# Kernel optimization log

Hardware: AMD Instinct MI355X
Metric: run time of the kernel (lower is better)

The kernel has to match this reference:

```python
import jax, jax.numpy as jnp
import numpy as np

B, C, L, H = 4, 512, 2048, 8
D = C // H  # head_dim


def setup_inputs() -> dict:
    key = jax.random.key(0)
    ks = jax.random.split(key, 9)
    s = 1.0 / np.sqrt(C)  # keep logits well-scaled like torch Linear init
    return {
        "x": jax.random.normal(ks[0], (B, C, L), dtype=jnp.float32),
        "Wq": jax.random.normal(ks[1], (C, C), dtype=jnp.float32) * s,
        "bq": jnp.zeros((C,), dtype=jnp.float32),
        "Wk": jax.random.normal(ks[2], (C, C), dtype=jnp.float32) * s,
        "bk": jnp.zeros((C,), dtype=jnp.float32),
        "Wv": jax.random.normal(ks[3], (C, C), dtype=jnp.float32) * s,
        "bv": jnp.zeros((C,), dtype=jnp.float32),
        "Wo": jax.random.normal(ks[4], (C, C), dtype=jnp.float32) * s,
        "bo": jnp.zeros((C,), dtype=jnp.float32),
    }


def reference(x, Wq, bq, Wk, bk, Wv, bv, Wo, bo):
    # x: (B, C, L) -> (B, L, C)
    xp = jnp.transpose(x, (0, 2, 1))
    scale = D ** (-0.5)

    def heads(w, b):
        y = xp @ w.T + b                      # (B, L, C)  torch Linear: x W^T + b
        return y.reshape(B, L, H, D).transpose(0, 2, 1, 3)  # (B, H, L, D)

    q = heads(Wq, bq)
    k = heads(Wk, bk)
    v = heads(Wv, bv)

    attn = jnp.einsum('bhqd,bhkd->bhqk', q, k) * scale  # (B, H, L, L)
    attn = jax.nn.softmax(attn, axis=-1)
    out = jnp.einsum('bhqk,bhkd->bhqd', attn, v)        # (B, H, L, D)
    out = out.transpose(0, 2, 1, 3).reshape(B, L, C)    # (B, L, C)
    out = out @ Wo.T + bo
    return x + jnp.transpose(out, (0, 2, 1))            # residual in (B, C, L)
```

## Files before the change

kernel.cpp:

```cpp
#include <hip/hip_runtime.h>
#include <math.h>

#define B_ 4
#define C_ 512
#define L_ 2048
#define H_ 8
#define D_ 64
#define QSCALE 0.18033688011112042f
#define DEFER_THR 12.0f

typedef __bf16 bf16x8 __attribute__((ext_vector_type(8)));
typedef float f32x4 __attribute__((ext_vector_type(4)));

__device__ __forceinline__ unsigned short f2bf(float f) {
    unsigned u = __float_as_uint(f);
    return (unsigned short)((u + 0x7FFFu + ((u >> 16) & 1u)) >> 16);
}
__device__ __forceinline__ unsigned pack2(float a, float b) {
    return (unsigned)f2bf(a) | ((unsigned)f2bf(b) << 16);
}
__device__ __forceinline__ bf16x8 frag_ld(const unsigned short* p) {
    uint4 v = *reinterpret_cast<const uint4*>(p);
    return __builtin_bit_cast(bf16x8, v);
}

__global__ __launch_bounds__(256) void transpose_conv(
    const float* __restrict__ x, unsigned short* __restrict__ xt)
{
    __shared__ float T[64][68];
    const int b  = blockIdx.z;
    const int l0 = blockIdx.x * 64;
    const int c0 = blockIdx.y * 64;
    const int t  = threadIdx.x;
    const float* xb = x + (size_t)b * C_ * L_;
    unsigned short* xtb = xt + (size_t)b * L_ * C_;

    #pragma unroll
    for (int p = 0; p < 4; ++p) {
        const int ci = 16 * p + (t >> 4);
        const int l4 = (t & 15) * 4;
        const float4 v = *reinterpret_cast<const float4*>(
            xb + (size_t)(c0 + ci) * L_ + l0 + l4);
        *reinterpret_cast<float4*>(&T[ci][l4]) = v;
    }
    __syncthreads();

    const int lo = t >> 2;
    const int cb = (t & 3) * 16;
    unsigned w[8];
    #pragma unroll
    for (int k = 0; k < 8; ++k)
        w[k] = pack2(T[cb + 2 * k][lo], T[cb + 2 * k + 1][lo]);
    unsigned short* dst = xtb + (size_t)(l0 + lo) * C_ + c0 + cb;
    *reinterpret_cast<uint4*>(dst)     = make_uint4(w[0], w[1], w[2], w[3]);
    *reinterpret_cast<uint4*>(dst + 8) = make_uint4(w[4], w[5], w[6], w[7]);
}

__global__ __launch_bounds__(256) void wconv(
    const float* __restrict__ w0, const float* __restrict__ w1,
    const float* __restrict__ w2, const float* __restrict__ w3,
    unsigned short* __restrict__ o0, unsigned short* __restrict__ o1,
    unsigned short* __restrict__ o2, unsigned short* __restrict__ o3)
{
    const int y = blockIdx.y;
    const float* src; unsigned short* dst;
    if      (y == 0) { src = w0; dst = o0; }
    else if (y == 1) { src = w1; dst = o1; }
    else if (y == 2) { src = w2; dst = o2; }
    else             { src = w3; dst = o3; }
    const size_t idx = ((size_t)blockIdx.x * 256 + threadIdx.x) * 4;
    const float4 v = *reinterpret_cast<const float4*>(src + idx);
    *reinterpret_cast<uint2*>(dst + idx) =
        make_uint2(pack2(v.x, v.y), pack2(v.z, v.w));
}

__global__ __launch_bounds__(256) void qkv_gemm(
    const unsigned short* __restrict__ xt,
    const unsigned short* __restrict__ wq, const unsigned short* __restrict__ wk,
    const unsigned short* __restrict__ wv,
    const float* __restrict__ bq, const float* __restrict__ bk,
    const float* __restrict__ bv,
    unsigned short* __restrict__ qb, unsigned short* __restrict__ kb,
    unsigned short* __restrict__ vb)
{
    __shared__ unsigned short As[128][40];
    __shared__ unsigned short Bs[128][40];

    const int mode = blockIdx.z >> 2;
    const int b    = blockIdx.z & 3;
    const size_t LC = (size_t)L_ * C_;

    const unsigned short *A, *Bt;
    const float* bias;
    unsigned short* Out;
    float scale = 1.0f;
    int m0, n0, oN, biasN;
    if (mode == 0) {
        A = xt + (size_t)b * LC; Bt = wq; bias = bq; Out = qb + (size_t)b * LC;
        m0 = blockIdx.y * 128; n0 = blockIdx.x * 128; oN = C_; biasN = 1;
        scale = QSCALE;
    } else if (mode == 1) {
        A = xt + (size_t)b * LC; Bt = wk; bias = bk; Out = kb + (size_t)b * LC;
        m0 = blockIdx.y * 128; n0 = blockIdx.x * 128; oN = C_; biasN = 1;
    } else {
        A = wv; Bt = xt + (size_t)b * LC; bias = bv; Out = vb + (size_t)b * LC;
        m0 = blockIdx.x * 128; n0 = blockIdx.y * 128; oN = L_; biasN = 0;
    }

    const int t = threadIdx.x;
    const int lane = t & 63, wid = t >> 6;
    const int wm = (wid >> 1) * 64, wn = (wid & 1) * 64;
    const int q16 = lane & 15, g = lane >> 4;

    const int srow = t >> 1;
    const int scol = (t & 1) * 16;
    const unsigned short* Ap = A  + (size_t)(m0 + srow) * C_ + scol;
    const unsigned short* Bp = Bt + (size_t)(n0 + srow) * C_ + scol;

    f32x4 zero4 = {0.f, 0.f, 0.f, 0.f};
    f32x4 acc[4][4];
    #pragma unroll
    for (int i = 0; i < 4; ++i)
        #pragma unroll
        for (int j = 0; j < 4; ++j) acc[i][j] = zero4;

    uint4 ar0 = *reinterpret_cast<const uint4*>(Ap);
    uint4 ar1 = *reinterpret_cast<const uint4*>(Ap + 8);
    uint4 br0 = *reinterpret_cast<const uint4*>(Bp);
    uint4 br1 = *reinterpret_cast<const uint4*>(Bp + 8);

    for (int k0 = 0; k0 < C_; k0 += 32) {
        __syncthreads();
        *reinterpret_cast<uint4*>(&As[srow][scol])     = ar0;
        *reinterpret_cast<uint4*>(&As[srow][scol + 8]) = ar1;
        *reinterpret_cast<uint4*>(&Bs[srow][scol])     = br0;
        *reinterpret_cast<uint4*>(&Bs[srow][scol + 8]) = br1;
        __syncthreads();
        if (k0 + 32 < C_) {
            ar0 = *reinterpret_cast<const uint4*>(Ap + k0 + 32);
            ar1 = *reinterpret_cast<const uint4*>(Ap + k0 + 40);
            br0 = *reinterpret_cast<const uint4*>(Bp + k0 + 32);
            br1 = *reinterpret_cast<const uint4*>(Bp + k0 + 40);
        }
        bf16x8 af[4], bfr[4];
        #pragma unroll
        for (int i = 0; i < 4; ++i) af[i]  = frag_ld(&As[wm + 16 * i + q16][8 * g]);
        #pragma unroll
        for (int j = 0; j < 4; ++j) bfr[j] = frag_ld(&Bs[wn + 16 * j + q16][8 * g]);
        #pragma unroll
        for (int i = 0; i < 4; ++i)
            #pragma unroll
            for (int j = 0; j < 4; ++j)
                acc[i][j] = __builtin_amdgcn_mfma_f32_16x16x32_bf16(
                    af[i], bfr[j], acc[i][j], 0, 0, 0);
    }

    #pragma unroll
    for (int j = 0; j < 4; ++j) {
        const int n = n0 + wn + 16 * j + q16;
        const float bn = biasN ? bias[n] : 0.f;
        #pragma unroll
        for (int i = 0; i < 4; ++i) {
            #pragma unroll
            for (int r = 0; r < 4; ++r) {
                const int m = m0 + wm + 16 * i + 4 * g + r;
                float v = acc[i][j][r] + (biasN ? bn : bias[m]);
                Out[(size_t)m * oN + n] = f2bf(v * scale);
            }
        }
    }
}

__global__ __launch_bounds__(256) void gemm_out(
    const unsigned short* __restrict__ A,
    const unsigned short* __restrict__ Bt,
    const float* __restrict__ bias,
    float* __restrict__ Out, const float* __restrict__ resid)
{
    __shared__ unsigned short As[128][40];
    __shared__ unsigned short Bs[128][40];

    const int bz = blockIdx.z;
    const size_t LC = (size_t)L_ * C_;
    Bt    += (size_t)bz * LC;
    Out   += (size_t)bz * LC;
    resid += (size_t)bz * LC;

    const int n0 = blockIdx.x * 128;
    const int m0 = blockIdx.y * 128;
    const int t  = threadIdx.x;
    const int lane = t & 63, wid = t >> 6;
    const int wm = (wid >> 1) * 64, wn = (wid & 1) * 64;
    const int q16 = lane & 15, g = lane >> 4;

    const int srow = t >> 1;
    const int scol = (t & 1) * 16;
    const unsigned short* Ap = A  + (size_t)(m0 + srow) * C_ + scol;
    const unsigned short* Bp = Bt + (size_t)(n0 + srow) * C_ + scol;

    f32x4 zero4 = {0.f, 0.f, 0.f, 0.f};
    f32x4 acc[4][4];
    #pragma unroll
    for (int i = 0; i < 4; ++i)
        #pragma unroll
        for (int j = 0; j < 4; ++j) acc[i][j] = zero4;

    uint4 ar0 = *reinterpret_cast<const uint4*>(Ap);
    uint4 ar1 = *reinterpret_cast<const uint4*>(Ap + 8);
    uint4 br0 = *reinterpret_cast<const uint4*>(Bp);
    uint4 br1 = *reinterpret_cast<const uint4*>(Bp + 8);

    for (int k0 = 0; k0 < C_; k0 += 32) {
        __syncthreads();
        *reinterpret_cast<uint4*>(&As[srow][scol])     = ar0;
        *reinterpret_cast<uint4*>(&As[srow][scol + 8]) = ar1;
        *reinterpret_cast<uint4*>(&Bs[srow][scol])     = br0;
        *reinterpret_cast<uint4*>(&Bs[srow][scol + 8]) = br1;
        __syncthreads();
        if (k0 + 32 < C_) {
            ar0 = *reinterpret_cast<const uint4*>(Ap + k0 + 32);
            ar1 = *reinterpret_cast<const uint4*>(Ap + k0 + 40);
            br0 = *reinterpret_cast<const uint4*>(Bp + k0 + 32);
            br1 = *reinterpret_cast<const uint4*>(Bp + k0 + 40);
        }
        bf16x8 af[4], bfr[4];
        #pragma unroll
        for (int i = 0; i < 4; ++i) af[i]  = frag_ld(&As[wm + 16 * i + q16][8 * g]);
        #pragma unroll
        for (int j = 0; j < 4; ++j) bfr[j] = frag_ld(&Bs[wn + 16 * j + q16][8 * g]);
        #pragma unroll
        for (int i = 0; i < 4; ++i)
            #pragma unroll
            for (int j = 0; j < 4; ++j)
                acc[i][j] = __builtin_amdgcn_mfma_f32_16x16x32_bf16(
                    af[i], bfr[j], acc[i][j], 0, 0, 0);
    }

    #pragma unroll
    for (int j = 0; j < 4; ++j) {
        const int n = n0 + wn + 16 * j + q16;
        #pragma unroll
        for (int i = 0; i < 4; ++i) {
            #pragma unroll
            for (int r = 0; r < 4; ++r) {
                const int m = m0 + wm + 16 * i + 4 * g + r;
                const size_t off = (size_t)m * L_ + n;
                Out[off] = acc[i][j][r] + bias[m] + resid[off];
            }
        }
    }
}

__global__ __launch_bounds__(256) void attn_mfma(
    const unsigned short* __restrict__ Qb,
    const unsigned short* __restrict__ Kb,
    const unsigned short* __restrict__ Vb,
    unsigned short* __restrict__ Ab)
{
    __shared__ unsigned short Ks[64][72];
    __shared__ unsigned short Vs[64][72];
    __shared__ unsigned short Pw[4][16][72];

    const int q0 = blockIdx.x * 64;
    const int h  = blockIdx.y;
    const int b  = blockIdx.z;
    const int t  = threadIdx.x, lane = t & 63, wid = t >> 6;
    const int q16 = lane & 15, g = lane >> 4;

    const unsigned short* Qg = Qb + (size_t)b * L_ * C_;
    const unsigned short* Kg = Kb + (size_t)b * L_ * C_;
    const unsigned short* Vg = Vb + ((size_t)b * C_ + h * D_) * L_;
    unsigned short* Ag       = Ab + (size_t)b * L_ * C_;

    bf16x8 qf[2];
    {
        const unsigned short* qp =
            Qg + (size_t)(q0 + 16 * wid + q16) * C_ + h * D_ + 8 * g;
        qf[0] = frag_ld(qp);
        qf[1] = frag_ld(qp + 32);
    }

    f32x4 zero4 = {0.f, 0.f, 0.f, 0.f};
    f32x4 oacc[4];
    #pragma unroll
    for (int n = 0; n < 4; ++n) oacc[n] = zero4;
    float m_s = -INFINITY;
    float l_s = 0.f;

    const int sr = t >> 2;
    const int sc = (t & 3) * 16;

    uint4 kr0, kr1, vr0, vr1;
    {
        const unsigned short* kp = Kg + (size_t)sr * C_ + h * D_ + sc;
        kr0 = *reinterpret_cast<const uint4*>(kp);
        kr1 = *reinterpret_cast<const uint4*>(kp + 8);
        const unsigned short* vp = Vg + (size_t)sr * L_ + sc;
        vr0 = *reinterpret_cast<const uint4*>(vp);
        vr1 = *reinterpret_cast<const uint4*>(vp + 8);
    }

    for (int kt = 0; kt < 32; ++kt) {
        __syncthreads();
        *reinterpret_cast<uint4*>(&Ks[sr][sc])     = kr0;
        *reinterpret_cast<uint4*>(&Ks[sr][sc + 8]) = kr1;
        *reinterpret_cast<uint4*>(&Vs[sr][sc])     = vr0;
        *reinterpret_cast<uint4*>(&Vs[sr][sc + 8]) = vr1;
        __syncthreads();
        if (kt + 1 < 32) {
            const int kn = (kt + 1) * 64;
            const unsigned short* kp = Kg + (size_t)(kn + sr) * C_ + h * D_ + sc;
            kr0 = *reinterpret_cast<const uint4*>(kp);
            kr1 = *reinterpret_cast<const uint4*>(kp + 8);
            const unsigned short* vp = Vg + (size_t)sr * L_ + kn + sc;
            vr0 = *reinterpret_cast<const uint4*>(vp);
            vr1 = *reinterpret_cast<const uint4*>(vp + 8);
        }

        f32x4 sacc[4];
        #pragma unroll
        for (int f = 0; f < 4; ++f) sacc[f] = zero4;
        #pragma unroll
        for (int s = 0; s < 2; ++s) {
            #pragma unroll
            for (int f = 0; f < 4; ++f) {
                bf16x8 kf = frag_ld(&Ks[16 * f + q16][32 * s + 8 * g]);
                sacc[f] = __builtin_amdgcn_mfma_f32_16x16x32_bf16(
                    kf, qf[s], sacc[f], 0, 0, 0);
            }
        }

        float fm[4];
        #pragma unroll
        for (int f = 0; f < 4; ++f)
            fm[f] = fmaxf(fmaxf(sacc[f][0], sacc[f][1]),
                          fmaxf(sacc[f][2], sacc[f][3]));
        float pm = fmaxf(fmaxf(fm[0], fm[1]), fmaxf(fm[2], fm[3]));
        pm = fmaxf(pm, __shfl_xor(pm, 16));
        pm = fmaxf(pm, __shfl_xor(pm, 32));

        if (!__all(pm - m_s <= DEFER_THR)) {
            const float mn   = fmaxf(m_s, pm);
            const float corr = exp2f(m_s - mn);
            m_s = mn;
            l_s *= corr;
            #pragma unroll
            for (int r = 0; r < 4; ++r) {
                const float c_o = __shfl(corr, 20 * g + r);
                #pragma unroll
                for (int n = 0; n < 4; ++n) oacc[n][r] *= c_o;
            }
        }

        float p[4][4];
        float fs[4];
        #pragma unroll
        for (int f = 0; f < 4; ++f) {
            #pragma unroll
            for (int r = 0; r < 4; ++r) p[f][r] = exp2f(sacc[f][r] - m_s);
            fs[f] = (p[f][0] + p[f][1]) + (p[f][2] + p[f][3]);
        }
        float rs = (fs[0] + fs[1]) + (fs[2] + fs[3]);
        rs += __shfl_xor(rs, 16);
        rs += __shfl_xor(rs, 32);
        l_s += rs;

        unsigned* pw = reinterpret_cast<unsigned*>(&Pw[wid][q16][0]);
        #pragma unroll
        for (int f = 0; f < 4; ++f) {
            pw[8 * f + 2 * g]     = pack2(p[f][0], p[f][1]);
            pw[8 * f + 2 * g + 1] = pack2(p[f][2], p[f][3]);
        }

        #pragma unroll
        for (int s2 = 0; s2 < 2; ++s2) {
            bf16x8 pf = frag_ld(&Pw[wid][q16][32 * s2 + 8 * g]);
            #pragma unroll
            for (int n = 0; n < 4; ++n) {
                bf16x8 vf = frag_ld(&Vs[16 * n + q16][32 * s2 + 8 * g]);
                oacc[n] = __builtin_amdgcn_mfma_f32_16x16x32_bf16(
                    pf, vf, oacc[n], 0, 0, 0);
            }
        }
    }

    #pragma unroll
    for (int r = 0; r < 4; ++r) {
        const float l_o = __shfl(l_s, 20 * g + r);
        const float inv = 1.f / l_o;
        const int q = q0 + 16 * wid + 4 * g + r;
        #pragma unroll
        for (int n = 0; n < 4; ++n)
            Ag[(size_t)q * C_ + h * D_ + 16 * n + q16] = f2bf(oacc[n][r] * inv);
    }
}

extern "C" void kernel_launch(void* const* d_in, const int* in_sizes, int n_in,
                              void* d_out, int out_size, void* d_ws, size_t ws_size,
                              hipStream_t stream)
{
    const float* x  = (const float*)d_in[0];
    const float* Wq = (const float*)d_in[1];
    const float* bq = (const float*)d_in[2];
    const float* Wk = (const float*)d_in[3];
    const float* bk = (const float*)d_in[4];
    const float* Wv = (const float*)d_in[5];
    const float* bv = (const float*)d_in[6];
    const float* Wo = (const float*)d_in[7];
    const float* bo = (const float*)d_in[8];
    float* out = (float*)d_out;

    const size_t NB = (size_t)B_ * L_ * C_;
    const size_t NW = (size_t)C_ * C_;
    unsigned short* ws16 = (unsigned short*)d_ws;
    unsigned short* xt  = ws16;
    unsigned short* qb  = xt  + NB;
    unsigned short* kb  = qb  + NB;
    unsigned short* vb  = kb  + NB;
    unsigned short* att = vb  + NB;
    unsigned short* wqb = att + NB;
    unsigned short* wkb = wqb + NW;
    unsigned short* wvb = wkb + NW;
    unsigned short* wob = wvb + NW;

    transpose_conv<<<dim3(L_ / 64, C_ / 64, B_), 256, 0, stream>>>(x, xt);
    wconv<<<dim3(256, 4), 256, 0, stream>>>(Wq, Wk, Wv, Wo, wqb, wkb, wvb, wob);

    qkv_gemm<<<dim3(4, 16, 3 * B_), 256, 0, stream>>>(
        xt, wqb, wkb, wvb, bq, bk, bv, qb, kb, vb);

    attn_mfma<<<dim3(L_ / 64, H_, B_), 256, 0, stream>>>(qb, kb, vb, att);

    gemm_out<<<dim3(16, 4, B_), 256, 0, stream>>>(wob, att, bo, out, x);
}
```

Before: 235.8 us.

## Fuse prep kernels, use direct-to-LDS loads, hardware bf16 convert, swizzled P buffer

Merges the transpose and weight-conversion kernels into one launch and swaps software bf16 rounding for the v_cvt_pk_bf16_f32 instruction. The QKV GEMM now stages tiles with global_load_lds straight into unpadded LDS instead of going through registers. In attention, the per-tile row-sum shuffle reduction moves to the end, and the P scratch buffer is XOR-swizzled instead of padded. The QKV GEMM loses its register prefetch overlap, so global load latency now sits on the critical path before each barrier, and unpadded LDS may bank-conflict on fragment reads.

```diff
diff --git a/kernel.cpp b/kernel.cpp
--- a/kernel.cpp
+++ b/kernel.cpp
@@ -12,66 +12,78 @@
 typedef __bf16 bf16x8 __attribute__((ext_vector_type(8)));
 typedef float f32x4 __attribute__((ext_vector_type(4)));
 
-__device__ __forceinline__ unsigned short f2bf(float f) {
-    unsigned u = __float_as_uint(f);
-    return (unsigned short)((u + 0x7FFFu + ((u >> 16) & 1u)) >> 16);
-}
-__device__ __forceinline__ unsigned pack2(float a, float b) {
-    return (unsigned)f2bf(a) | ((unsigned)f2bf(b) << 16);
+__device__ __forceinline__ unsigned cvt_pk(float lo, float hi) {
+    unsigned r;
+    asm("v_cvt_pk_bf16_f32 %0, %1, %2" : "=v"(r) : "v"(lo), "v"(hi));
+    return r;
+}
+__device__ __forceinline__ unsigned short f2bf_hw(float a) {
+    unsigned r;
+    asm("v_cvt_pk_bf16_f32 %0, %1, %1" : "=v"(r) : "v"(a));
+    return (unsigned short)r;
 }
 __device__ __forceinline__ bf16x8 frag_ld(const unsigned short* p) {
     uint4 v = *reinterpret_cast<const uint4*>(p);
     return __builtin_bit_cast(bf16x8, v);
 }
-
-__global__ __launch_bounds__(256) void transpose_conv(
-    const float* __restrict__ x, unsigned short* __restrict__ xt)
-{
-    __shared__ float T[64][68];
-    const int b  = blockIdx.z;
-    const int l0 = blockIdx.x * 64;
-    const int c0 = blockIdx.y * 64;
-    const int t  = threadIdx.x;
-    const float* xb = x + (size_t)b * C_ * L_;
-    unsigned short* xtb = xt + (size_t)b * L_ * C_;
-
-    #pragma unroll
-    for (int p = 0; p < 4; ++p) {
-        const int ci = 16 * p + (t >> 4);
-        const int l4 = (t & 15) * 4;
-        const float4 v = *reinterpret_cast<const float4*>(
-            xb + (size_t)(c0 + ci) * L_ + l0 + l4);
-        *reinterpret_cast<float4*>(&T[ci][l4]) = v;
-    }
-    __syncthreads();
-
-    const int lo = t >> 2;
-    const int cb = (t & 3) * 16;
-    unsigned w[8];
-    #pragma unroll
-    for (int k = 0; k < 8; ++k)
-        w[k] = pack2(T[cb + 2 * k][lo], T[cb + 2 * k + 1][lo]);
-    unsigned short* dst = xtb + (size_t)(l0 + lo) * C_ + c0 + cb;
-    *reinterpret_cast<uint4*>(dst)     = make_uint4(w[0], w[1], w[2], w[3]);
-    *reinterpret_cast<uint4*>(dst + 8) = make_uint4(w[4], w[5], w[6], w[7]);
-}
-
-__global__ __launch_bounds__(256) void wconv(
+__device__ __forceinline__ float fmax3(float a, float b, float c) {
+    return fmaxf(fmaxf(a, b), c);
+}
+__device__ __forceinline__ void glds16(const void* g, void* l) {
+    __builtin_amdgcn_global_load_lds(
+        (const __attribute__((address_space(1))) void*)g,
+        (__attribute__((address_space(3))) void*)l, 16, 0, 0);
+}
+
+__global__ __launch_bounds__(256) void prep(
+    const float* __restrict__ x,
     const float* __restrict__ w0, const float* __restrict__ w1,
     const float* __restrict__ w2, const float* __restrict__ w3,
+    unsigned short* __restrict__ xt,
     unsigned short* __restrict__ o0, unsigned short* __restrict__ o1,
     unsigned short* __restrict__ o2, unsigned short* __restrict__ o3)
 {
-    const int y = blockIdx.y;
-    const float* src; unsigned short* dst;
-    if      (y == 0) { src = w0; dst = o0; }
-    else if (y == 1) { src = w1; dst = o1; }
-    else if (y == 2) { src = w2; dst = o2; }
-    else             { src = w3; dst = o3; }
-    const size_t idx = ((size_t)blockIdx.x * 256 + threadIdx.x) * 4;
-    const float4 v = *reinterpret_cast<const float4*>(src + idx);
-    *reinterpret_cast<uint2*>(dst + idx) =
-        make_uint2(pack2(v.x, v.y), pack2(v.z, v.w));
+    __shared__ float T[64][68];
+    const int t = threadIdx.x;
+
+    if (blockIdx.z < B_) {
+        const int b  = blockIdx.z;
+        const int l0 = blockIdx.x * 64;
+        const int c0 = blockIdx.y * 64;
+        const float* xb = x + (size_t)b * C_ * L_;
+        unsigned short* xtb = xt + (size_t)b * L_ * C_;
+
+        #pragma unroll
+        for (int p = 0; p < 4; ++p) {
+            const int ci = 16 * p + (t >> 4);
+            const int l4 = (t & 15) * 4;
+            *reinterpret_cast<float4*>(&T[ci][l4]) =
+                *reinterpret_cast<const float4*>(xb + (size_t)(c0 + ci) * L_ + l0 + l4);
+        }
+        __syncthreads();
+
+        const int lo = t >> 2;
+        const int cb = (t & 3) * 16;
+        unsigned w[8];
+        #pragma unroll
+        for (int k = 0; k < 8; ++k)
+            w[k] = cvt_pk(T[cb + 2 * k][lo], T[cb + 2 * k + 1][lo]);
+        unsigned short* dst = xtb + (size_t)(l0 + lo) * C_ + c0 + cb;
+        *reinterpret_cast<uint4*>(dst)     = make_uint4(w[0], w[1], w[2], w[3]);
+        *reinterpret_cast<uint4*>(dst + 8) = make_uint4(w[4], w[5], w[6], w[7]);
+    } else {
+        const int m = blockIdx.z - B_;
+        const float* src; unsigned short* dst;
+        if      (m == 0) { src = w0; dst = o0; }
+        else if (m == 1) { src = w1; dst = o1; }
+        else if (m == 2) { src = w2; dst = o2; }
+        else             { src = w3; dst = o3; }
+        const int flat = blockIdx.x + 32 * blockIdx.y;
+        const size_t idx = ((size_t)flat * 256 + t) * 4;
+        const float4 v = *reinterpret_cast<const float4*>(src + idx);
+        *reinterpret_cast<uint2*>(dst + idx) =
+            make_uint2(cvt_pk(v.x, v.y), cvt_pk(v.z, v.w));
+    }
 }
 
 __global__ __launch_bounds__(256) void qkv_gemm(
@@ -83,8 +95,8 @@
     unsigned short* __restrict__ qb, unsigned short* __restrict__ kb,
     unsigned short* __restrict__ vb)
 {
-    __shared__ unsigned short As[128][40];
-    __shared__ unsigned short Bs[128][40];
+    __shared__ unsigned short As[128][32];
+    __shared__ unsigned short Bs[128][32];
 
     const int mode = blockIdx.z >> 2;
     const int b    = blockIdx.z & 3;
@@ -112,10 +124,16 @@
     const int wm = (wid >> 1) * 64, wn = (wid & 1) * 64;
     const int q16 = lane & 15, g = lane >> 4;
 
-    const int srow = t >> 1;
-    const int scol = (t & 1) * 16;
-    const unsigned short* Ap = A  + (size_t)(m0 + srow) * C_ + scol;
-    const unsigned short* Bp = Bt + (size_t)(n0 + srow) * C_ + scol;
+    const int gr = wid * 32 + (lane >> 2);
+    const int gc = (lane & 3) * 8;
+    const unsigned short* Ap0 = A  + (size_t)(m0 + gr) * C_ + gc;
+    const unsigned short* Ap1 = Ap0 + 16 * C_;
+    const unsigned short* Bp0 = Bt + (size_t)(n0 + gr) * C_ + gc;
+    const unsigned short* Bp1 = Bp0 + 16 * C_;
+    unsigned short* lA0 = &As[wid * 32][0];
+    unsigned short* lA1 = &As[wid * 32 + 16][0];
+    unsigned short* lB0 = &Bs[wid * 32][0];
+    unsigned short* lB1 = &Bs[wid * 32 + 16][0];
 
     f32x4 zero4 = {0.f, 0.f, 0.f, 0.f};
     f32x4 acc[4][4];
@@ -124,24 +142,11 @@
         #pragma unroll
         for (int j = 0; j < 4; ++j) acc[i][j] = zero4;
 
-    uint4 ar0 = *reinterpret_cast<const uint4*>(Ap);
-    uint4 ar1 = *reinterpret_cast<const uint4*>(Ap + 8);
-    uint4 br0 = *reinterpret_cast<const uint4*>(Bp);
-    uint4 br1 = *reinterpret_cast<const uint4*>(Bp + 8);
-
     for (int k0 = 0; k0 < C_; k0 += 32) {
         __syncthreads();
-        *reinterpret_cast<uint4*>(&As[srow][scol])     = ar0;
-        *reinterpret_cast<uint4*>(&As[srow][scol + 8]) = ar1;
-        *reinterpret_cast<uint4*>(&Bs[srow][scol])     = br0;
-        *reinterpret_cast<uint4*>(&Bs[srow][scol + 8]) = br1;
-        __syncthreads();
-        if (k0 + 32 < C_) {
-            ar0 = *reinterpret_cast<const uint4*>(Ap + k0 + 32);
-            ar1 = *reinterpret_cast<const uint4*>(Ap + k0 + 40);
-            br0 = *reinterpret_cast<const uint4*>(Bp + k0 + 32);
-            br1 = *reinterpret_cast<const uint4*>(Bp + k0 + 40);
-        }
+        glds16(Ap0 + k0, lA0); glds16(Ap1 + k0, lA1);
+        glds16(Bp0 + k0, lB0); glds16(Bp1 + k0, lB1);
+        __syncthreads();
         bf16x8 af[4], bfr[4];
         #pragma unroll
         for (int i = 0; i < 4; ++i) af[i]  = frag_ld(&As[wm + 16 * i + q16][8 * g]);
@@ -164,8 +169,8 @@
             #pragma unroll
             for (int r = 0; r < 4; ++r) {
                 const int m = m0 + wm + 16 * i + 4 * g + r;
-                float v = acc[i][j][r] + (biasN ? bn : bias[m]);
-                Out[(size_t)m * oN + n] = f2bf(v * scale);
+                const float v = acc[i][j][r] + (biasN ? bn : bias[m]);
+                Out[(size_t)m * oN + n] = f2bf_hw(v * scale);
             }
         }
     }
@@ -259,18 +264,21 @@
 {
     __shared__ unsigned short Ks[64][72];
     __shared__ unsigned short Vs[64][72];
-    __shared__ unsigned short Pw[4][16][72];
+    __shared__ unsigned short Pw[4][16][64];
 
     const int q0 = blockIdx.x * 64;
     const int h  = blockIdx.y;
     const int b  = blockIdx.z;
     const int t  = threadIdx.x, lane = t & 63, wid = t >> 6;
     const int q16 = lane & 15, g = lane >> 4;
+    const int h4 = (q16 & 7) << 2;
 
     const unsigned short* Qg = Qb + (size_t)b * L_ * C_;
     const unsigned short* Kg = Kb + (size_t)b * L_ * C_;
     const unsigned short* Vg = Vb + ((size_t)b * C_ + h * D_) * L_;
     unsigned short* Ag       = Ab + (size_t)b * L_ * C_;
+
+    unsigned* pw = reinterpret_cast<unsigned*>(&Pw[wid][q16][0]);
 
     bf16x8 qf[2];
     {
@@ -285,7 +293,7 @@
     #pragma unroll
     for (int n = 0; n < 4; ++n) oacc[n] = zero4;
     float m_s = -INFINITY;
-    float l_s = 0.f;
+    float l_p = 0.f;
 
     const int sr = t >> 2;
     const int sc = (t & 3) * 16;
@@ -330,12 +338,12 @@
             }
         }
 
-        float fm[4];
-        #pragma unroll
-        for (int f = 0; f < 4; ++f)
-            fm[f] = fmaxf(fmaxf(sacc[f][0], sacc[f][1]),
-                          fmaxf(sacc[f][2], sacc[f][3]));
-        float pm = fmaxf(fmaxf(fm[0], fm[1]), fmaxf(fm[2], fm[3]));
+        const float t0 = fmax3(sacc[0][0], sacc[0][1], sacc[0][2]);
+        const float t1 = fmax3(sacc[0][3], sacc[1][0], sacc[1][1]);
+        const float t2 = fmax3(sacc[1][2], sacc[1][3], sacc[2][0]);
+        const float t3 = fmax3(sacc[2][1], sacc[2][2], sacc[2][3]);
+        const float t4 = fmax3(sacc[3][0], sacc[3][1], sacc[3][2]);
+        float pm = fmaxf(fmax3(t0, t1, t2), fmax3(t3, t4, sacc[3][3]));
         pm = fmaxf(pm, __shfl_xor(pm, 16));
         pm = fmaxf(pm, __shfl_xor(pm, 32));
 
@@ -343,7 +351,7 @@
             const float mn   = fmaxf(m_s, pm);
             const float corr = exp2f(m_s - mn);
             m_s = mn;
-            l_s *= corr;
+            l_p *= corr;
             #pragma unroll
             for (int r = 0; r < 4; ++r) {
                 const float c_o = __shfl(corr, 20 * g + r);
@@ -353,28 +361,25 @@
         }
 
         float p[4][4];
-        float fs[4];
         #pragma unroll
         for (int f = 0; f < 4; ++f) {
             #pragma unroll
             for (int r = 0; r < 4; ++r) p[f][r] = exp2f(sacc[f][r] - m_s);
-            fs[f] = (p[f][0] + p[f][1]) + (p[f][2] + p[f][3]);
-        }
-        float rs = (fs[0] + fs[1]) + (fs[2] + fs[3]);
-        rs += __shfl_xor(rs, 16);
-        rs += __shfl_xor(rs, 32);
-        l_s += rs;
-
-        unsigned* pw = reinterpret_cast<unsigned*>(&Pw[wid][q16][0]);
+            l_p += (p[f][0] + p[f][1]) + (p[f][2] + p[f][3]);
+        }
+
         #pragma unroll
         for (int f = 0; f < 4; ++f) {
-            pw[8 * f + 2 * g]     = pack2(p[f][0], p[f][1]);
-            pw[8 * f + 2 * g + 1] = pack2(p[f][2], p[f][3]);
+            uint2 v2;
+            v2.x = cvt_pk(p[f][0], p[f][1]);
+            v2.y = cvt_pk(p[f][2], p[f][3]);
+            *reinterpret_cast<uint2*>(pw + ((8 * f + 2 * g) ^ h4)) = v2;
         }
 
         #pragma unroll
         for (int s2 = 0; s2 < 2; ++s2) {
-            bf16x8 pf = frag_ld(&Pw[wid][q16][32 * s2 + 8 * g]);
+            bf16x8 pf = frag_ld(reinterpret_cast<const unsigned short*>(
+                pw + ((16 * s2 + 4 * g) ^ h4)));
             #pragma unroll
             for (int n = 0; n < 4; ++n) {
                 bf16x8 vf = frag_ld(&Vs[16 * n + q16][32 * s2 + 8 * g]);
@@ -384,14 +389,17 @@
         }
     }
 
+    float lr = l_p;
+    lr += __shfl_xor(lr, 16);
+    lr += __shfl_xor(lr, 32);
     #pragma unroll
     for (int r = 0; r < 4; ++r) {
-        const float l_o = __shfl(l_s, 20 * g + r);
+        const float l_o = __shfl(lr, 20 * g + r);
         const float inv = 1.f / l_o;
         const int q = q0 + 16 * wid + 4 * g + r;
         #pragma unroll
         for (int n = 0; n < 4; ++n)
-            Ag[(size_t)q * C_ + h * D_ + 16 * n + q16] = f2bf(oacc[n][r] * inv);
+            Ag[(size_t)q * C_ + h * D_ + 16 * n + q16] = f2bf_hw(oacc[n][r] * inv);
     }
 }
 
@@ -423,8 +431,8 @@
     unsigned short* wvb = wkb + NW;
     unsigned short* wob = wvb + NW;
 
-    transpose_conv<<<dim3(L_ / 64, C_ / 64, B_), 256, 0, stream>>>(x, xt);
-    wconv<<<dim3(256, 4), 256, 0, stream>>>(Wq, Wk, Wv, Wo, wqb, wkb, wvb, wob);
+    prep<<<dim3(32, 8, 2 * B_), 256, 0, stream>>>(
+        x, Wq, Wk, Wv, Wo, xt, wqb, wkb, wvb, wob);
 
     qkv_gemm<<<dim3(4, 16, 3 * B_), 256, 0, stream>>>(
         xt, wqb, wkb, wvb, bq, bk, bv, qb, kb, vb);
```

Measured after the change: 211.1 us. 1.12x faster.
